# Kernel optimization log

Measured on AMD Instinct MI355X. Metric: run time of the kernel, lower is better.

## Reference

```python
import jax, jax.numpy as jnp
import numpy as np

G = 7  # grid size hardcoded in the original loops


def _xyxy(t, off, m, n):
    # t: (B, C, G, G); channels off..off+3 are (x_off, y_off, w, h)
    cx = (t[:, off + 0] + m) / G
    cy = (t[:, off + 1] + n) / G
    w = t[:, off + 2]
    h = t[:, off + 3]
    return cx - w / 2, cy - h / 2, cx + w / 2, cy + h / 2


def _iou(a, b):
    ix1 = jnp.maximum(a[0], b[0])
    iy1 = jnp.maximum(a[1], b[1])
    ix2 = jnp.minimum(a[2], b[2])
    iy2 = jnp.minimum(a[3], b[3])
    inter = jnp.maximum(ix2 - ix1, 0.0) * jnp.maximum(iy2 - iy1, 0.0)
    area_a = (a[2] - a[0]) * (a[3] - a[1])
    area_b = (b[2] - b[0]) * (b[3] - b[1])
    return jnp.where(inter > 0, inter / (area_a + area_b - inter), 0.0)


def setup_inputs() -> dict:
    key = jax.random.key(0)
    k1, k2, k3 = jax.random.split(key, 3)
    B = 8192
    pred = jax.random.uniform(k1, (B, 30, G, G), dtype=jnp.float32)
    labels = jax.random.uniform(k2, (B, 30, G, G), dtype=jnp.float32)
    # objectness channel must be exactly 1.0 for cells containing objects
    obj = (jax.random.uniform(k3, (B, G, G)) < 0.3).astype(jnp.float32)
    labels = labels.at[:, 4].set(obj)
    return {"pred": pred, "labels": labels}


def reference(pred, labels):
    B = pred.shape[0]
    dt = pred.dtype
    m = jnp.arange(G, dtype=dt)[:, None]  # index along dim -2 (as in loop var m)
    n = jnp.arange(G, dtype=dt)[None, :]  # index along dim -1 (loop var n)

    b1 = _xyxy(pred, 0, m, n)
    b2 = _xyxy(pred, 5, m, n)
    gt = _xyxy(labels, 0, m, n)
    iou1 = _iou(b1, gt)  # (B, G, G)
    iou2 = _iou(b2, gt)
    use1 = iou1 >= iou2
    obj = labels[:, 4] == 1.0

    coor1 = (jnp.sum((pred[:, 0:2] - labels[:, 0:2]) ** 2, axis=1)
             + jnp.sum((jnp.sqrt(pred[:, 2:4]) - jnp.sqrt(labels[:, 2:4])) ** 2, axis=1))
    coor2 = (jnp.sum((pred[:, 5:7] - labels[:, 5:7]) ** 2, axis=1)
             + jnp.sum((jnp.sqrt(pred[:, 7:9]) - jnp.sqrt(labels[:, 7:9])) ** 2, axis=1))
    coor = 5.0 * jnp.where(use1, coor1, coor2)

    e1 = (pred[:, 4] - iou1) ** 2
    e2 = (pred[:, 9] - iou2) ** 2
    obj_conf = jnp.where(use1, e1, e2)
    noobj_conf_objcell = 0.5 * jnp.where(use1, e2, e1)
    noobj_conf_nocell = 0.5 * (pred[:, 4] ** 2 + pred[:, 9] ** 2)

    cls = jnp.sum((pred[:, 10:] - labels[:, 10:]) ** 2, axis=1)

    per_cell = jnp.where(obj,
                         coor + obj_conf + noobj_conf_objcell + cls,
                         noobj_conf_nocell)
    return jnp.sum(per_cell) / B
```

## Files before the change

### kernel.cpp

```cpp
#include <hip/hip_runtime.h>

#define GDIM 7
#define CELLS 49
#define CH 30
#define BLK 256

__device__ __forceinline__ float iou_fn(float ax1, float ay1, float ax2, float ay2,
                                        float bx1, float by1, float bx2, float by2) {
    float ix1 = fmaxf(ax1, bx1);
    float iy1 = fmaxf(ay1, by1);
    float ix2 = fminf(ax2, bx2);
    float iy2 = fminf(ay2, by2);
    float iw = fmaxf(ix2 - ix1, 0.0f);
    float ih = fmaxf(iy2 - iy1, 0.0f);
    float inter = iw * ih;
    float aa = (ax2 - ax1) * (ay2 - ay1);
    float ab = (bx2 - bx1) * (by2 - by1);
    return inter > 0.0f ? inter / (aa + ab - inter) : 0.0f;
}

__global__ __launch_bounds__(BLK) void yolo_stage1(const float* __restrict__ pred,
                                                   const float* __restrict__ lab,
                                                   float* __restrict__ partial,
                                                   int total_cells) {
    int i = blockIdx.x * BLK + threadIdx.x;
    float per_cell = 0.0f;
    if (i < total_cells) {
        int b = i / CELLS;
        int cell = i - b * CELLS;
        int mr = cell / GDIM;
        int nc = cell - mr * GDIM;
        const float* p = pred + (size_t)b * (CH * CELLS) + cell;
        const float* l = lab  + (size_t)b * (CH * CELLS) + cell;

        float pv[10], lv[10];
        #pragma unroll
        for (int c = 0; c < 10; ++c) pv[c] = p[c * CELLS];
        #pragma unroll
        for (int c = 0; c < 10; ++c) lv[c] = l[c * CELLS];

        float cls = 0.0f;
        #pragma unroll
        for (int c = 10; c < CH; ++c) {
            float d = p[c * CELLS] - l[c * CELLS];
            cls = fmaf(d, d, cls);
        }

        float fm = (float)mr, fn = (float)nc;

        float gcx = (lv[0] + fm) / 7.0f;
        float gcy = (lv[1] + fn) / 7.0f;
        float gx1 = gcx - lv[2] * 0.5f, gy1 = gcy - lv[3] * 0.5f;
        float gx2 = gcx + lv[2] * 0.5f, gy2 = gcy + lv[3] * 0.5f;

        float c1x = (pv[0] + fm) / 7.0f;
        float c1y = (pv[1] + fn) / 7.0f;
        float b1x1 = c1x - pv[2] * 0.5f, b1y1 = c1y - pv[3] * 0.5f;
        float b1x2 = c1x + pv[2] * 0.5f, b1y2 = c1y + pv[3] * 0.5f;

        float c2x = (pv[5] + fm) / 7.0f;
        float c2y = (pv[6] + fn) / 7.0f;
        float b2x1 = c2x - pv[7] * 0.5f, b2y1 = c2y - pv[8] * 0.5f;
        float b2x2 = c2x + pv[7] * 0.5f, b2y2 = c2y + pv[8] * 0.5f;

        float iou1 = iou_fn(b1x1, b1y1, b1x2, b1y2, gx1, gy1, gx2, gy2);
        float iou2 = iou_fn(b2x1, b2y1, b2x2, b2y2, gx1, gy1, gx2, gy2);
        bool use1 = iou1 >= iou2;

        float d0 = pv[0] - lv[0], d1 = pv[1] - lv[1];
        float s2 = sqrtf(pv[2]) - sqrtf(lv[2]);
        float s3 = sqrtf(pv[3]) - sqrtf(lv[3]);
        float coor1 = d0 * d0 + d1 * d1 + s2 * s2 + s3 * s3;

        float d5 = pv[5] - lv[5], d6 = pv[6] - lv[6];
        float s7 = sqrtf(pv[7]) - sqrtf(lv[7]);
        float s8 = sqrtf(pv[8]) - sqrtf(lv[8]);
        float coor2 = d5 * d5 + d6 * d6 + s7 * s7 + s8 * s8;

        float coor = 5.0f * (use1 ? coor1 : coor2);

        float e1 = pv[4] - iou1; e1 *= e1;
        float e2 = pv[9] - iou2; e2 *= e2;
        float obj_conf   = use1 ? e1 : e2;
        float noobj_obj  = 0.5f * (use1 ? e2 : e1);
        float noobj_none = 0.5f * (pv[4] * pv[4] + pv[9] * pv[9]);

        bool obj = (lv[4] == 1.0f);
        per_cell = obj ? (coor + obj_conf + noobj_obj + cls) : noobj_none;
    }

    float v = per_cell;
    #pragma unroll
    for (int off = 32; off > 0; off >>= 1) v += __shfl_down(v, off, 64);

    __shared__ float sdata[BLK / 64];
    int lane = threadIdx.x & 63;
    int wid  = threadIdx.x >> 6;
    if (lane == 0) sdata[wid] = v;
    __syncthreads();
    if (threadIdx.x == 0) {
        float s = 0.0f;
        #pragma unroll
        for (int w = 0; w < BLK / 64; ++w) s += sdata[w];
        partial[blockIdx.x] = s;
    }
}

__global__ __launch_bounds__(BLK) void yolo_stage2(const float* __restrict__ partial,
                                                   int n, float inv_b,
                                                   float* __restrict__ out) {
    float v = 0.0f;
    for (int i = threadIdx.x; i < n; i += BLK) v += partial[i];
    #pragma unroll
    for (int off = 32; off > 0; off >>= 1) v += __shfl_down(v, off, 64);

    __shared__ float sdata[BLK / 64];
    int lane = threadIdx.x & 63;
    int wid  = threadIdx.x >> 6;
    if (lane == 0) sdata[wid] = v;
    __syncthreads();
    if (threadIdx.x == 0) {
        float s = 0.0f;
        #pragma unroll
        for (int w = 0; w < BLK / 64; ++w) s += sdata[w];
        out[0] = s * inv_b;
    }
}

extern "C" void kernel_launch(void* const* d_in, const int* in_sizes, int n_in,
                              void* d_out, int out_size, void* d_ws, size_t ws_size,
                              hipStream_t stream) {
    const float* pred = (const float*)d_in[0];
    const float* lab  = (const float*)d_in[1];
    int B = in_sizes[0] / (CH * CELLS);
    int total_cells = B * CELLS;
    int nblocks = (total_cells + BLK - 1) / BLK;

    float* partial = (float*)d_ws;
    float* out = (float*)d_out;

    yolo_stage1<<<nblocks, BLK, 0, stream>>>(pred, lab, partial, total_cells);
    yolo_stage2<<<1, BLK, 0, stream>>>(partial, nblocks, 1.0f / (float)B, out);
}
```

Measured before the change: 25.75 us.

## Stage batches in LDS with vector loads and fuse final reduction via atomic counter

Each block now loads four whole batch images of pred and labels into shared memory with float4 loads, then computes per-cell losses from LDS. The separate second reduction kernel is replaced by a last-block-done pattern using an atomic counter reset by a memset. This aims to improve load efficiency and remove a kernel launch, at the cost of large LDS use per block (lower occupancy), idle threads (196 of 256 compute), and an added memset.

Result: slower. 70.99 us (+175.7%).

```diff
diff --git a/kernel.cpp b/kernel.cpp
--- a/kernel.cpp
+++ b/kernel.cpp
@@ -3,7 +3,10 @@
 #define GDIM 7
 #define CELLS 49
 #define CH 30
+#define FPB (CH * CELLS)
+#define BPB 4
 #define BLK 256
+#define LDSF (BPB * FPB)
 
 __device__ __forceinline__ float iou_fn(float ax1, float ay1, float ax2, float ay2,
                                         float bx1, float by1, float bx2, float by2) {
@@ -19,19 +22,49 @@
     return inter > 0.0f ? inter / (aa + ab - inter) : 0.0f;
 }
 
-__global__ __launch_bounds__(BLK) void yolo_stage1(const float* __restrict__ pred,
-                                                   const float* __restrict__ lab,
-                                                   float* __restrict__ partial,
-                                                   int total_cells) {
-    int i = blockIdx.x * BLK + threadIdx.x;
+__global__ __launch_bounds__(BLK) void yolo_fused(const float* __restrict__ pred,
+                                                  const float* __restrict__ lab,
+                                                  float* __restrict__ partial,
+                                                  unsigned int* __restrict__ counter,
+                                                  float* __restrict__ out,
+                                                  int B, int nblocks, float inv_b) {
+    __shared__ float sp[LDSF];
+    __shared__ float sl[LDSF];
+    __shared__ float swave[BLK / 64];
+    __shared__ int s_last;
+
+    const int tid = threadIdx.x;
+    const int b0 = blockIdx.x * BPB;
+    int nb = B - b0;
+    if (nb > BPB) nb = BPB;
+
+    const size_t base = (size_t)b0 * FPB;
+    if (nb == BPB) {
+        const float4* pg = (const float4*)(pred + base);
+        const float4* lg = (const float4*)(lab + base);
+        float4* sp4 = (float4*)sp;
+        float4* sl4 = (float4*)sl;
+        for (int i = tid; i < LDSF / 4; i += BLK) {
+            sp4[i] = pg[i];
+            sl4[i] = lg[i];
+        }
+    } else {
+        const int nf = nb * FPB;
+        for (int i = tid; i < nf; i += BLK) {
+            sp[i] = pred[base + i];
+            sl[i] = lab[base + i];
+        }
+    }
+    __syncthreads();
+
     float per_cell = 0.0f;
-    if (i < total_cells) {
-        int b = i / CELLS;
-        int cell = i - b * CELLS;
-        int mr = cell / GDIM;
-        int nc = cell - mr * GDIM;
-        const float* p = pred + (size_t)b * (CH * CELLS) + cell;
-        const float* l = lab  + (size_t)b * (CH * CELLS) + cell;
+    if (tid < nb * CELLS) {
+        const int b = tid / CELLS;
+        const int cell = tid - b * CELLS;
+        const int mr = cell / GDIM;
+        const int nc = cell - mr * GDIM;
+        const float* p = sp + b * FPB + cell;
+        const float* l = sl + b * FPB + cell;
 
         float pv[10], lv[10];
         #pragma unroll
@@ -46,7 +79,7 @@
             cls = fmaf(d, d, cls);
         }
 
-        float fm = (float)mr, fn = (float)nc;
+        const float fm = (float)mr, fn = (float)nc;
 
         float gcx = (lv[0] + fm) / 7.0f;
         float gcy = (lv[1] + fn) / 7.0f;
@@ -93,37 +126,36 @@
     #pragma unroll
     for (int off = 32; off > 0; off >>= 1) v += __shfl_down(v, off, 64);
 
-    __shared__ float sdata[BLK / 64];
-    int lane = threadIdx.x & 63;
-    int wid  = threadIdx.x >> 6;
-    if (lane == 0) sdata[wid] = v;
+    const int lane = tid & 63;
+    const int wid = tid >> 6;
+    if (lane == 0) swave[wid] = v;
     __syncthreads();
-    if (threadIdx.x == 0) {
+    if (tid == 0) {
         float s = 0.0f;
         #pragma unroll
-        for (int w = 0; w < BLK / 64; ++w) s += sdata[w];
+        for (int w = 0; w < BLK / 64; ++w) s += swave[w];
         partial[blockIdx.x] = s;
+        __threadfence();
+        unsigned int prev = atomicAdd(counter, 1u);
+        s_last = (prev == (unsigned int)(nblocks - 1)) ? 1 : 0;
     }
-}
+    __syncthreads();
 
-__global__ __launch_bounds__(BLK) void yolo_stage2(const float* __restrict__ partial,
-                                                   int n, float inv_b,
-                                                   float* __restrict__ out) {
-    float v = 0.0f;
-    for (int i = threadIdx.x; i < n; i += BLK) v += partial[i];
-    #pragma unroll
-    for (int off = 32; off > 0; off >>= 1) v += __shfl_down(v, off, 64);
-
-    __shared__ float sdata[BLK / 64];
-    int lane = threadIdx.x & 63;
-    int wid  = threadIdx.x >> 6;
-    if (lane == 0) sdata[wid] = v;
-    __syncthreads();
-    if (threadIdx.x == 0) {
-        float s = 0.0f;
+    if (s_last) {
+        __threadfence();
+        float t = 0.0f;
+        for (int i = tid; i < nblocks; i += BLK) t += partial[i];
         #pragma unroll
-        for (int w = 0; w < BLK / 64; ++w) s += sdata[w];
-        out[0] = s * inv_b;
+        for (int off = 32; off > 0; off >>= 1) t += __shfl_down(t, off, 64);
+        __syncthreads();
+        if (lane == 0) swave[wid] = t;
+        __syncthreads();
+        if (tid == 0) {
+            float s = 0.0f;
+            #pragma unroll
+            for (int w = 0; w < BLK / 64; ++w) s += swave[w];
+            out[0] = s * inv_b;
+        }
     }
 }
 
@@ -132,13 +164,14 @@
                               hipStream_t stream) {
     const float* pred = (const float*)d_in[0];
     const float* lab  = (const float*)d_in[1];
-    int B = in_sizes[0] / (CH * CELLS);
-    int total_cells = B * CELLS;
-    int nblocks = (total_cells + BLK - 1) / BLK;
+    int B = in_sizes[0] / FPB;
+    int nblocks = (B + BPB - 1) / BPB;
 
     float* partial = (float*)d_ws;
+    unsigned int* counter = (unsigned int*)((char*)d_ws + (64 * 1024));
     float* out = (float*)d_out;
 
-    yolo_stage1<<<nblocks, BLK, 0, stream>>>(pred, lab, partial, total_cells);
-    yolo_stage2<<<1, BLK, 0, stream>>>(partial, nblocks, 1.0f / (float)B, out);
+    hipMemsetAsync(counter, 0, sizeof(unsigned int), stream);
+    yolo_fused<<<nblocks, BLK, 0, stream>>>(pred, lab, partial, counter, out,
+                                            B, nblocks, 1.0f / (float)B);
 }
```
